# Kernel optimization log

Measured on AMD Instinct MI355X. Metric: run time of the kernel, lower is better.

Reference implementation:

```python
import jax, jax.numpy as jnp
import numpy as np

B, L, D, H = 8, 1024, 1024, 16
DH = D // H  # 64


def setup_inputs() -> dict:
    key = jax.random.key(0)
    ks = jax.random.split(key, 6)
    x = jax.random.normal(ks[0], (B, L, D), dtype=jnp.float32)
    mask = jax.random.randint(ks[1], (1, L, L), 0, 2).astype(jnp.float32)
    # params initialized ~ normal(std=0.1) as in the module's _initialize
    Wk = jax.random.normal(ks[2], (D, D), dtype=jnp.float32) * 0.1
    Wv = jax.random.normal(ks[3], (D, D), dtype=jnp.float32) * 0.1
    Wq = jax.random.normal(ks[4], (D, D), dtype=jnp.float32) * 0.1
    Wo = jax.random.normal(ks[5], (D, D), dtype=jnp.float32) * 0.1
    return {"x": x, "mask": mask, "Wk": Wk, "Wv": Wv, "Wq": Wq, "Wo": Wo}


def reference(x, mask, Wk, Wv, Wq, Wo):
    # torch Linear: y = x @ W.T
    k = jnp.einsum('bld,ed->ble', x, Wk).reshape(B, L, H, DH)
    v = jnp.einsum('bld,ed->ble', x, Wv).reshape(B, L, H, DH)
    q = jnp.einsum('bld,ed->ble', x, Wq).reshape(B, L, H, DH)
    # explicit score matrix [B, H, L, L]
    scores = jnp.einsum('blhe,bmhe->bhlm', q, k)
    m = mask[:, None]  # (1, 1, L, L) broadcasts over batch and heads
    scores = scores * m - 1e9 * (1.0 - m)
    scale = np.float32(1.0 / np.sqrt(DH))
    weights = jax.nn.softmax(scores * scale, axis=-1)
    out = jnp.einsum('bhlm,bmhe->blhe', weights, v).reshape(B, L, D)
    out = jnp.einsum('bld,ed->ble', out, Wo)  # output_linear (n_heads > 1)
    return out
```

## Files before the change

kernel.cpp:

```cpp
#include <hip/hip_runtime.h>

#define B_  8
#define L_  1024
#define D_  1024
#define H_  16
#define DH_ 64

typedef unsigned short u16;
typedef __attribute__((ext_vector_type(8))) short short8;
typedef __attribute__((ext_vector_type(8))) _Float16 half8;
typedef __attribute__((ext_vector_type(4))) float floatx4;
typedef __attribute__((ext_vector_type(16))) float floatx16;

static __device__ __forceinline__ u16 f2bf(float f) {
  union { float f; unsigned u; } cv; cv.f = f;
  unsigned u = cv.u;
  return (u16)((u + 0x7fffu + ((u >> 16) & 1u)) >> 16);
}
static __device__ __forceinline__ u16 f2h(float f) {
  union { _Float16 h; u16 u; } cv; cv.h = (_Float16)f; return cv.u;
}
static __device__ __forceinline__ unsigned pack_bf2(float a, float b) {
  union { float f; unsigned u; } ua, ub; ua.f = a; ub.f = b;
  return __builtin_amdgcn_perm(ub.u + 0x8000u, ua.u + 0x8000u, 0x07060302u);
}

#if __has_builtin(__builtin_amdgcn_exp2f)
#define EXP2(x) __builtin_amdgcn_exp2f(x)
#else
#define EXP2(x) __expf((x) * 0.6931471805599453f)
#endif

__global__ void cast_all(const float* __restrict__ x,  const float* __restrict__ wq,
                         const float* __restrict__ wk, const float* __restrict__ wv,
                         const float* __restrict__ wo, const float* __restrict__ mask,
                         u16* __restrict__ xf,  u16* __restrict__ wqf,
                         u16* __restrict__ wkf, u16* __restrict__ wvf,
                         u16* __restrict__ wof, float* __restrict__ biasP) {
  int blk = blockIdx.x;
  if (blk >= 12288) {
    int i = (blk - 12288) * 256 + threadIdx.x;
    int e = i & 3, lane = (i >> 2) & 63, rr = (i >> 8) & 3, t = (i >> 10) & 1;
    int c = (i >> 11) & 15, w = (i >> 15) & 3, qt = i >> 17;
    int kk  = e + 8 * rr + 4 * (lane >> 5);
    int row = qt * 128 + w * 32 + (lane & 31);
    int key = c * 64 + t * 32 + kk;
    biasP[i] = (mask[(size_t)row * L_ + key] - 1.0f) * 1.8033688e8f - 34.624681f;
    return;
  }
  const float* src; u16* dst; int off;
  if (blk < 8192)       { src = x;  dst = xf;  off = blk; }
  else if (blk < 9216)  { src = wq; dst = wqf; off = blk - 8192; }
  else if (blk < 10240) { src = wk; dst = wkf; off = blk - 9216; }
  else if (blk < 11264) { src = wv; dst = wvf; off = blk - 10240; }
  else                  { src = wo; dst = wof; off = blk - 11264; }
  int i = off * 1024 + threadIdx.x * 4;
  float4 f = *(const float4*)(src + i);
  ushort4 r;
  r.x = f2h(f.x); r.y = f2h(f.y); r.z = f2h(f.z); r.w = f2h(f.w);
  *(ushort4*)(dst + i) = r;
}

typedef __attribute__((address_space(3))) void  lds_void;
typedef const __attribute__((address_space(1))) void g_void;
static __device__ __forceinline__ void load_lds16(const void* g, void* l) {
  __builtin_amdgcn_global_load_lds((g_void*)g, (lds_void*)l, 16, 0, 0);
}

__global__ __launch_bounds__(256) void gemm_qkv(const u16* __restrict__ A,
                                                const u16* __restrict__ wq,
                                                const u16* __restrict__ wk,
                                                const u16* __restrict__ wv,
                                                u16* __restrict__ qf,
                                                u16* __restrict__ kf,
                                                u16* __restrict__ vb) {
  const int K = D_, N = D_;
  int nb = blockIdx.x;
  const u16* Bw; u16* Cp; float scale; int obf;
  if (nb < 8)       { Bw = wq; Cp = qf; scale = 0.18033688f; obf = 0; }
  else if (nb < 16) { Bw = wk; Cp = kf; scale = 1.0f;        obf = 0; }
  else              { Bw = wv; Cp = vb; scale = 1.0f;        obf = 1; }
  const int n0 = (nb & 7) * 128;

  __shared__ u16 lA[128 * 32];
  __shared__ u16 lB[128 * 32];
  const int tid  = threadIdx.x;
  const int w    = tid >> 6;
  const int lane = tid & 63;
  const int m    = lane & 15;
  const int kg   = lane >> 4;
  const int m0   = blockIdx.y * 128;
  const int wm   = (w >> 1) * 64;
  const int wn   = (w & 1) * 64;
  const int rowS = tid >> 2;
  const int part = tid & 3;

  floatx4 acc[4][4];
#pragma unroll
  for (int i = 0; i < 4; ++i)
#pragma unroll
    for (int j = 0; j < 4; ++j)
#pragma unroll
      for (int r = 0; r < 4; ++r) acc[i][j][r] = 0.0f;

  for (int k0 = 0; k0 < K; k0 += 32) {
    __syncthreads();
#pragma unroll
    for (int rnd = 0; rnd < 2; ++rnd) {
      const u16* ga = A  + (size_t)(m0 + rnd * 64 + rowS) * K + k0 + part * 8;
      const u16* gb = Bw + (size_t)(n0 + rnd * 64 + rowS) * K + k0 + part * 8;
      load_lds16(ga, lA + rnd * 2048 + w * 512);
      load_lds16(gb, lB + rnd * 2048 + w * 512);
    }
    __syncthreads();

    half8 af[4], bf[4];
#pragma unroll
    for (int i = 0; i < 4; ++i) af[i] = *(const half8*)&lA[(wm + i * 16 + m) * 32 + kg * 8];
#pragma unroll
    for (int i = 0; i < 4; ++i) bf[i] = *(const half8*)&lB[(wn + i * 16 + m) * 32 + kg * 8];
#pragma unroll
    for (int mi = 0; mi < 4; ++mi)
#pragma unroll
      for (int ni = 0; ni < 4; ++ni)
        acc[mi][ni] = __builtin_amdgcn_mfma_f32_16x16x32_f16(af[mi], bf[ni], acc[mi][ni], 0, 0, 0);
  }

#pragma unroll
  for (int mi = 0; mi < 4; ++mi)
#pragma unroll
    for (int ni = 0; ni < 4; ++ni)
#pragma unroll
      for (int r = 0; r < 4; ++r) {
        int row = m0 + wm + mi * 16 + kg * 4 + r;
        int col = n0 + wn + ni * 16 + m;
        size_t idx = (size_t)row * N + col;
        float vv = acc[mi][ni][r] * scale;
        Cp[idx] = obf ? f2bf(vv) : f2h(vv);
      }
}

__global__ __launch_bounds__(256) void gemm_fin(const u16* __restrict__ A,
                                                const u16* __restrict__ Bw,
                                                float* __restrict__ Cp,
                                                int M, int N, int K) {
  __shared__ u16 lA[128 * 32];
  __shared__ u16 lB[128 * 32];
  const int tid  = threadIdx.x;
  const int w    = tid >> 6;
  const int lane = tid & 63;
  const int m    = lane & 15;
  const int kg   = lane >> 4;
  const int m0   = blockIdx.y * 128;
  const int n0   = blockIdx.x * 128;
  const int wm   = (w >> 1) * 64;
  const int wn   = (w & 1) * 64;
  const int rowS = tid >> 2;
  const int part = tid & 3;

  floatx4 acc[4][4];
#pragma unroll
  for (int i = 0; i < 4; ++i)
#pragma unroll
    for (int j = 0; j < 4; ++j)
#pragma unroll
      for (int r = 0; r < 4; ++r) acc[i][j][r] = 0.0f;

  for (int k0 = 0; k0 < K; k0 += 32) {
    __syncthreads();
#pragma unroll
    for (int rnd = 0; rnd < 2; ++rnd) {
      const u16* ga = A  + (size_t)(m0 + rnd * 64 + rowS) * K + k0 + part * 8;
      const u16* gb = Bw + (size_t)(n0 + rnd * 64 + rowS) * K + k0 + part * 8;
      load_lds16(ga, lA + rnd * 2048 + w * 512);
      load_lds16(gb, lB + rnd * 2048 + w * 512);
    }
    __syncthreads();

    half8 af[4], bf[4];
#pragma unroll
    for (int i = 0; i < 4; ++i) af[i] = *(const half8*)&lA[(wm + i * 16 + m) * 32 + kg * 8];
#pragma unroll
    for (int i = 0; i < 4; ++i) bf[i] = *(const half8*)&lB[(wn + i * 16 + m) * 32 + kg * 8];
#pragma unroll
    for (int mi = 0; mi < 4; ++mi)
#pragma unroll
      for (int ni = 0; ni < 4; ++ni)
        acc[mi][ni] = __builtin_amdgcn_mfma_f32_16x16x32_f16(af[mi], bf[ni], acc[mi][ni], 0, 0, 0);
  }

#pragma unroll
  for (int mi = 0; mi < 4; ++mi)
#pragma unroll
    for (int ni = 0; ni < 4; ++ni)
#pragma unroll
      for (int r = 0; r < 4; ++r) {
        int row = m0 + wm + mi * 16 + kg * 4 + r;
        int col = n0 + wn + ni * 16 + m;
        Cp[(size_t)row * N + col] = acc[mi][ni][r];
      }
}

__global__ __launch_bounds__(256) void transpose_v(const u16* __restrict__ v,
                                                   u16* __restrict__ vt) {
  __shared__ u16 lds[64][72];
  const int b  = blockIdx.y >> 4;
  const int h  = blockIdx.y & 15;
  const int l0 = blockIdx.x * 64;
  const int tid = threadIdx.x;
#pragma unroll
  for (int it = 0; it < 2; ++it) {
    int idx = it * 256 + tid;
    int i = idx >> 3, off = (idx & 7) * 8;
    *(short8*)&lds[i][off] =
        *(const short8*)(v + ((size_t)(b * L_ + l0 + i)) * D_ + h * 64 + off);
  }
  __syncthreads();
  const int j  = tid >> 2;
  const int p0 = (tid & 3) * 16;
  __attribute__((aligned(16))) u16 tmp[16];
#pragma unroll
  for (int s = 0; s < 16; ++s) {
    int p = p0 + s;
    int l = (p >> 1) + ((p & 1) << 5);
    tmp[s] = lds[l][j];
  }
  u16* dst = vt + ((size_t)((b * H_ + h) * DH_ + j)) * L_ + l0 + p0;
  *(short8*)(dst)     = *(const short8*)&tmp[0];
  *(short8*)(dst + 8) = *(const short8*)&tmp[8];
}

__global__ __launch_bounds__(256, 4) void attn_kernel(const u16* __restrict__ q,
                                                      const u16* __restrict__ k,
                                                      const u16* __restrict__ vt,
                                                      const float* __restrict__ biasP,
                                                      u16* __restrict__ o) {
  __shared__ u16 lK[64][72];
  __shared__ u16 lVt[64][72];
  __shared__ float lRS[4][32];

  const int bh = blockIdx.x, qt = blockIdx.y;
  const int b = bh >> 4, h = bh & 15;
  const int tid = threadIdx.x;
  const int w = tid >> 6, lane = tid & 63;
  const int c32 = lane & 31, hi = lane >> 5;
  const int qr0 = qt * 128 + w * 32;

  const int srow  = tid >> 3;
  const int skoff = (tid & 7) * 8;

  const size_t qbase = ((size_t)((b * L_ + qr0 + c32) * H_ + h)) * DH_;
  half8 aq[4];
#pragma unroll
  for (int ks = 0; ks < 4; ++ks)
    aq[ks] = *(const half8*)(q + qbase + ks * 16 + hi * 8);

  floatx16 acc0, acc1;
#pragma unroll
  for (int i = 0; i < 16; ++i) { acc0[i] = 0.0f; acc1[i] = 0.0f; }
  float rsum0 = 0.0f, rsum1 = 0.0f;

  const u16* kp = k  + ((size_t)((b * L_ + srow) * H_ + h)) * DH_ + skoff;
  const u16* vp = vt + ((size_t)((b * H_ + h) * DH_ + srow)) * L_ + skoff;

  short8 rk[2], rv[2];
#pragma unroll
  for (int it = 0; it < 2; ++it) {
    rk[it] = *(const short8*)(kp + (size_t)it * 32 * H_ * DH_);
    rv[it] = *(const short8*)(vp + (size_t)it * 32 * L_);
  }

  const float4* bp = (const float4*)(biasP + ((size_t)(qt * 4 + w) * 16) * 2048) + lane;

  for (int c = 0; c < 16; ++c) {
    __syncthreads();
#pragma unroll
    for (int it = 0; it < 2; ++it) {
      *(short8*)&lK[it * 32 + srow][skoff]  = rk[it];
      *(short8*)&lVt[it * 32 + srow][skoff] = rv[it];
    }
    __syncthreads();

    floatx16 s0, s1;
#pragma unroll
    for (int rr = 0; rr < 4; ++rr) {
      float4 b0 = bp[rr * 64];
      float4 b1 = bp[(4 + rr) * 64];
      s0[rr * 4 + 0] = b0.x; s0[rr * 4 + 1] = b0.y; s0[rr * 4 + 2] = b0.z; s0[rr * 4 + 3] = b0.w;
      s1[rr * 4 + 0] = b1.x; s1[rr * 4 + 1] = b1.y; s1[rr * 4 + 2] = b1.z; s1[rr * 4 + 3] = b1.w;
    }
    bp += 512;

    if (c < 15) {
      kp += (size_t)64 * H_ * DH_;
      vp += 64;
#pragma unroll
      for (int it = 0; it < 2; ++it) {
        rk[it] = *(const short8*)(kp + (size_t)it * 32 * H_ * DH_);
        rv[it] = *(const short8*)(vp + (size_t)it * 32 * L_);
      }
    }

#pragma unroll
    for (int ks = 0; ks < 4; ++ks) {
      half8 bk0 = *(const half8*)&lK[c32][ks * 16 + hi * 8];
      half8 bk1 = *(const half8*)&lK[32 + c32][ks * 16 + hi * 8];
      s0 = __builtin_amdgcn_mfma_f32_32x32x16_f16(bk0, aq[ks], s0, 0, 0, 0);
      s1 = __builtin_amdgcn_mfma_f32_32x32x16_f16(bk1, aq[ks], s1, 0, 0, 0);
    }

    union { short8 v[4]; unsigned u[16]; } ap;
#pragma unroll
    for (int reg = 0; reg < 16; ++reg) {
      float p0 = EXP2(s0[reg]);
      float p1 = EXP2(s1[reg]);
      ap.u[reg] = pack_bf2(p0, p1);
      if (reg & 1) rsum1 += p0 + p1; else rsum0 += p0 + p1;
    }

#pragma unroll
    for (int ks = 0; ks < 4; ++ks) {
      short8 bv0 = *(const short8*)&lVt[c32][ks * 16 + hi * 8];
      short8 bv1 = *(const short8*)&lVt[32 + c32][ks * 16 + hi * 8];
      acc0 = __builtin_amdgcn_mfma_f32_32x32x16_bf16(ap.v[ks], bv0, acc0, 0, 0, 0);
      acc1 = __builtin_amdgcn_mfma_f32_32x32x16_bf16(ap.v[ks], bv1, acc1, 0, 0, 0);
    }
  }

  float rsum = rsum0 + rsum1;
  rsum += __shfl_xor(rsum, 32, 64);
  if (hi == 0) lRS[w][c32] = rsum;

#pragma unroll
  for (int reg = 0; reg < 16; ++reg) {
    int rl = (reg & 3) + 8 * (reg >> 2) + 4 * hi;
    float inv = 1.0f / lRS[w][rl];
    int row = qr0 + rl;
    size_t obase = ((size_t)((b * L_ + row) * H_ + h)) * DH_;
    o[obase + c32]      = f2h(acc0[reg] * inv);
    o[obase + 32 + c32] = f2h(acc1[reg] * inv);
  }
}

extern "C" void kernel_launch(void* const* d_in, const int* in_sizes, int n_in,
                              void* d_out, int out_size, void* d_ws, size_t ws_size,
                              hipStream_t stream) {
  const float* x    = (const float*)d_in[0];
  const float* mask = (const float*)d_in[1];
  const float* Wk   = (const float*)d_in[2];
  const float* Wv   = (const float*)d_in[3];
  const float* Wq   = (const float*)d_in[4];
  const float* Wo   = (const float*)d_in[5];

  char* ws = (char*)d_ws;
  u16* xf    = (u16*)(ws);
  u16* aout  = xf;
  u16* kf    = (u16*)(ws + (16ull << 20));
  u16* vtb   = (u16*)(ws + (32ull << 20));
  float* biasP = (float*)(ws + (48ull << 20));
  u16* wqf   = (u16*)(ws + (52ull << 20));
  u16* wkf   = (u16*)(ws + (54ull << 20));
  u16* wvf   = (u16*)(ws + (56ull << 20));
  u16* wof   = (u16*)(ws + (58ull << 20));
  u16* qf = (u16*)d_out;
  u16* vb = qf + (size_t)B_ * L_ * D_;

  cast_all<<<16384, 256, 0, stream>>>(x, Wq, Wk, Wv, Wo, mask,
                                      xf, wqf, wkf, wvf, wof, biasP);

  gemm_qkv<<<dim3(24, 64), 256, 0, stream>>>(xf, wqf, wkf, wvf, qf, kf, vb);

  transpose_v<<<dim3(L_ / 64, B_ * H_), 256, 0, stream>>>(vb, vtb);

  attn_kernel<<<dim3(B_ * H_, L_ / 128), 256, 0, stream>>>(qf, kf, vtb, biasP, aout);

  gemm_fin<<<dim3(D_ / 128, (B_ * L_) / 128), 256, 0, stream>>>(
      aout, wof, (float*)d_out, B_ * L_, D_, D_);
}
```

Before: 254.7 us.

## Double-buffer LDS tiles and XOR-swizzle layout in QKV and output GEMMs

Both projection GEMMs now keep two LDS buffers and prefetch the tile two steps ahead with direct global-to-LDS loads. Explicit vmcnt waits and barriers replace the two __syncthreads per iteration, so global loads overlap the MFMA work. The LDS column chunks are XOR-swizzled by row to cut bank conflicts on the half8 fragment reads. This doubles LDS use and depends on hand-counted vmcnt values being correct for the load count.

After: 255.1 us. Within noise of the previous version (+0.1%).

```diff
diff --git a/kernel.cpp b/kernel.cpp
--- a/kernel.cpp
+++ b/kernel.cpp
@@ -82,8 +82,8 @@
   else              { Bw = wv; Cp = vb; scale = 1.0f;        obf = 1; }
   const int n0 = (nb & 7) * 128;
 
-  __shared__ u16 lA[128 * 32];
-  __shared__ u16 lB[128 * 32];
+  __shared__ u16 lA[2 * 128 * 32];
+  __shared__ u16 lB[2 * 128 * 32];
   const int tid  = threadIdx.x;
   const int w    = tid >> 6;
   const int lane = tid & 63;
@@ -94,6 +94,8 @@
   const int wn   = (w & 1) * 64;
   const int rowS = tid >> 2;
   const int part = tid & 3;
+  const int csrc8 = ((part ^ ((rowS >> 1) & 3))) * 8;
+  const int kgs   = (kg ^ ((m >> 1) & 3)) * 8;
 
   floatx4 acc[4][4];
 #pragma unroll
@@ -103,27 +105,42 @@
 #pragma unroll
       for (int r = 0; r < 4; ++r) acc[i][j][r] = 0.0f;
 
+  auto STAGE = [&](int k0, int bufsel) {
+#pragma unroll
+    for (int rnd = 0; rnd < 2; ++rnd) {
+      const u16* ga = A  + (size_t)(m0 + rnd * 64 + rowS) * K + k0 + csrc8;
+      const u16* gb = Bw + (size_t)(n0 + rnd * 64 + rowS) * K + k0 + csrc8;
+      load_lds16(ga, lA + bufsel * 4096 + rnd * 2048 + w * 512);
+      load_lds16(gb, lB + bufsel * 4096 + rnd * 2048 + w * 512);
+    }
+  };
+
+  STAGE(0, 0);
+  STAGE(32, 1);
+
   for (int k0 = 0; k0 < K; k0 += 32) {
-    __syncthreads();
-#pragma unroll
-    for (int rnd = 0; rnd < 2; ++rnd) {
-      const u16* ga = A  + (size_t)(m0 + rnd * 64 + rowS) * K + k0 + part * 8;
-      const u16* gb = Bw + (size_t)(n0 + rnd * 64 + rowS) * K + k0 + part * 8;
-      load_lds16(ga, lA + rnd * 2048 + w * 512);
-      load_lds16(gb, lB + rnd * 2048 + w * 512);
-    }
-    __syncthreads();
-
+    const int buf = (k0 >> 5) & 1;
+    if (k0 + 32 < K) { asm volatile("s_waitcnt vmcnt(4)" ::: "memory"); }
+    else             { asm volatile("s_waitcnt vmcnt(0)" ::: "memory"); }
+    __builtin_amdgcn_s_barrier();
+    __builtin_amdgcn_sched_barrier(0);
+
+    const u16* pA = lA + buf * 4096;
+    const u16* pB = lB + buf * 4096;
     half8 af[4], bf[4];
 #pragma unroll
-    for (int i = 0; i < 4; ++i) af[i] = *(const half8*)&lA[(wm + i * 16 + m) * 32 + kg * 8];
-#pragma unroll
-    for (int i = 0; i < 4; ++i) bf[i] = *(const half8*)&lB[(wn + i * 16 + m) * 32 + kg * 8];
+    for (int i = 0; i < 4; ++i) af[i] = *(const half8*)&pA[(wm + i * 16 + m) * 32 + kgs];
+#pragma unroll
+    for (int i = 0; i < 4; ++i) bf[i] = *(const half8*)&pB[(wn + i * 16 + m) * 32 + kgs];
 #pragma unroll
     for (int mi = 0; mi < 4; ++mi)
 #pragma unroll
       for (int ni = 0; ni < 4; ++ni)
         acc[mi][ni] = __builtin_amdgcn_mfma_f32_16x16x32_f16(af[mi], bf[ni], acc[mi][ni], 0, 0, 0);
+
+    __builtin_amdgcn_sched_barrier(0);
+    __builtin_amdgcn_s_barrier();
+    if (k0 + 64 < K) STAGE(k0 + 64, buf);
   }
 
 #pragma unroll
@@ -144,8 +161,8 @@
                                                 const u16* __restrict__ Bw,
                                                 float* __restrict__ Cp,
                                                 int M, int N, int K) {
-  __shared__ u16 lA[128 * 32];
-  __shared__ u16 lB[128 * 32];
+  __shared__ u16 lA[2 * 128 * 32];
+  __shared__ u16 lB[2 * 128 * 32];
   const int tid  = threadIdx.x;
   const int w    = tid >> 6;
   const int lane = tid & 63;
@@ -157,6 +174,8 @@
   const int wn   = (w & 1) * 64;
   const int rowS = tid >> 2;
   const int part = tid & 3;
+  const int csrc8 = ((part ^ ((rowS >> 1) & 3))) * 8;
+  const int kgs   = (kg ^ ((m >> 1) & 3)) * 8;
 
   floatx4 acc[4][4];
 #pragma unroll
@@ -166,27 +185,42 @@
 #pragma unroll
       for (int r = 0; r < 4; ++r) acc[i][j][r] = 0.0f;
 
+  auto STAGE = [&](int k0, int bufsel) {
+#pragma unroll
+    for (int rnd = 0; rnd < 2; ++rnd) {
+      const u16* ga = A  + (size_t)(m0 + rnd * 64 + rowS) * K + k0 + csrc8;
+      const u16* gb = Bw + (size_t)(n0 + rnd * 64 + rowS) * K + k0 + csrc8;
+      load_lds16(ga, lA + bufsel * 4096 + rnd * 2048 + w * 512);
+      load_lds16(gb, lB + bufsel * 4096 + rnd * 2048 + w * 512);
+    }
+  };
+
+  STAGE(0, 0);
+  STAGE(32, 1);
+
   for (int k0 = 0; k0 < K; k0 += 32) {
-    __syncthreads();
-#pragma unroll
-    for (int rnd = 0; rnd < 2; ++rnd) {
-      const u16* ga = A  + (size_t)(m0 + rnd * 64 + rowS) * K + k0 + part * 8;
-      const u16* gb = Bw + (size_t)(n0 + rnd * 64 + rowS) * K + k0 + part * 8;
-      load_lds16(ga, lA + rnd * 2048 + w * 512);
-      load_lds16(gb, lB + rnd * 2048 + w * 512);
-    }
-    __syncthreads();
-
+    const int buf = (k0 >> 5) & 1;
+    if (k0 + 32 < K) { asm volatile("s_waitcnt vmcnt(4)" ::: "memory"); }
+    else             { asm volatile("s_waitcnt vmcnt(0)" ::: "memory"); }
+    __builtin_amdgcn_s_barrier();
+    __builtin_amdgcn_sched_barrier(0);
+
+    const u16* pA = lA + buf * 4096;
+    const u16* pB = lB + buf * 4096;
     half8 af[4], bf[4];
 #pragma unroll
-    for (int i = 0; i < 4; ++i) af[i] = *(const half8*)&lA[(wm + i * 16 + m) * 32 + kg * 8];
-#pragma unroll
-    for (int i = 0; i < 4; ++i) bf[i] = *(const half8*)&lB[(wn + i * 16 + m) * 32 + kg * 8];
+    for (int i = 0; i < 4; ++i) af[i] = *(const half8*)&pA[(wm + i * 16 + m) * 32 + kgs];
+#pragma unroll
+    for (int i = 0; i < 4; ++i) bf[i] = *(const half8*)&pB[(wn + i * 16 + m) * 32 + kgs];
 #pragma unroll
     for (int mi = 0; mi < 4; ++mi)
 #pragma unroll
       for (int ni = 0; ni < 4; ++ni)
         acc[mi][ni] = __builtin_amdgcn_mfma_f32_16x16x32_f16(af[mi], bf[ni], acc[mi][ni], 0, 0, 0);
+
+    __builtin_amdgcn_sched_barrier(0);
+    __builtin_amdgcn_s_barrier();
+    if (k0 + 64 < K) STAGE(k0 + 64, buf);
   }
 
 #pragma unroll
```
